# Performance work log

Measured on AMD Instinct MI355X. Metric: run time of the kernel, lower is better.

Reference implementation:

```python
import jax, jax.numpy as jnp
import numpy as np

B, N = 64, 4096          # trees per batch, leaves per complete binary tree
V, S = 21, 50            # amino-acid vocab, grammar-symbol vocab
E, H = 64, 128           # embed_dim, hidden_dim


def setup_inputs() -> dict:
    key = jax.random.key(0)
    ks = jax.random.split(key, 16)

    def lin_w(k, din, dout):
        return (jax.random.normal(k, (dout, din), jnp.float32) / np.sqrt(din)).astype(jnp.float32)

    tokens = jax.random.randint(ks[0], (B, N), 0, V, dtype=jnp.int32)
    symbols = jax.random.randint(ks[1], (B, N - 1), 0, S, dtype=jnp.int32)

    emb = jax.random.normal(ks[2], (V, E), jnp.float32) * 0.02
    emb = emb.at[0].set(0.0)  # padding_idx=0
    sym_emb = jax.random.normal(ks[3], (S, E), jnp.float32) * 0.02

    return {
        "tokens": tokens, "symbols": symbols,
        "emb": emb, "sym_emb": sym_emb,
        "Wp": lin_w(ks[4], E, H), "bp": jnp.zeros((H,), jnp.float32),
        "Wi": lin_w(ks[5], H, H), "bi": jnp.zeros((H,), jnp.float32),
        "Ui": lin_w(ks[6], H, H),
        "Wf": lin_w(ks[7], H, H), "bf": jnp.zeros((H,), jnp.float32),
        "Uf": lin_w(ks[8], H, H),
        "Wo": lin_w(ks[9], H, H), "bo": jnp.zeros((H,), jnp.float32),
        "Uo": lin_w(ks[10], H, H),
        "Wu": lin_w(ks[11], H, H), "bu": jnp.zeros((H,), jnp.float32),
        "Uu": lin_w(ks[12], H, H),
        "Wout": lin_w(ks[13], H, H), "bout": jnp.zeros((H,), jnp.float32),
    }


def _encode(tokens, symbols, emb, sym_emb, Wp, bp, Wi, bi, Ui, Wf, bf, Uf,
            Wo, bo, Uo, Wu, bu, Uu, Wout, bout):
    emb = emb.at[0].set(0.0)  # padding row contributes nothing (and gets no grad)

    # Leaf nodes: amino-acid embedding -> input_proj, no children.
    x = emb[tokens] @ Wp.T + bp                      # [B, N, H]
    i = jax.nn.sigmoid(x @ Wi.T + bi)
    o = jax.nn.sigmoid(x @ Wo.T + bo)
    u = jnp.tanh(x @ Wu.T + bu)
    c = i * u                                        # [B, N, H]
    h = o * jnp.tanh(c)

    # Bottom-up over levels of the complete binary tree (Child-Sum Tree-LSTM).
    off, n = 0, N
    while n > 1:
        m = n // 2
        xs = sym_emb[symbols[:, off:off + m]] @ Wp.T + bp   # [B, m, H]
        hl, hr = h[:, 0::2], h[:, 1::2]
        cl, cr = c[:, 0::2], c[:, 1::2]
        ht = hl + hr                                         # h_tilde = sum_j h_j
        gi = jax.nn.sigmoid(xs @ Wi.T + bi + ht @ Ui.T)
        go = jax.nn.sigmoid(xs @ Wo.T + bo + ht @ Uo.T)
        gu = jnp.tanh(xs @ Wu.T + bu + ht @ Uu.T)
        fx = xs @ Wf.T + bf
        fl = jax.nn.sigmoid(fx + hl @ Uf.T)                  # per-child forget gates
        fr = jax.nn.sigmoid(fx + hr @ Uf.T)
        c = gi * gu + fl * cl + fr * cr
        h = go * jnp.tanh(c)
        off += m
        n = m

    root_h = h[:, 0]                                         # [B, H]
    return root_h @ Wout.T + bout                            # output_proj


def reference(tokens, symbols, emb, sym_emb, Wp, bp, Wi, bi, Ui, Wf, bf, Uf,
              Wo, bo, Uo, Wu, bu, Uu, Wout, bout):
    return _encode(tokens, symbols, emb, sym_emb, Wp, bp, Wi, bi, Ui, Wf, bf,
                   Uf, Wo, bo, Uo, Wu, bu, Uu, Wout, bout)
```

## Files before the change

### kernel.cpp

```cpp
#include <hip/hip_runtime.h>
#include <hip/hip_bf16.h>

typedef __attribute__((ext_vector_type(8))) short short8;
typedef __attribute__((ext_vector_type(4))) float f32x4;

static constexpr int B_ = 64;
static constexpr int N_ = 4096;
static constexpr int V_ = 21;
static constexpr int S_ = 50;
static constexpr int E_ = 64;
static constexpr int H_ = 128;
static constexpr int NPAIR = V_ * V_;
static constexpr int NTAB = NPAIR * S_;

__device__ __forceinline__ float rcp_(float x) { return __builtin_amdgcn_rcpf(x); }
__device__ __forceinline__ float sigm(float x) { return rcp_(1.0f + __expf(-x)); }
__device__ __forceinline__ float tanh_(float x) {
  float a = fabsf(x);
  float e = __expf(-2.0f * a);
  float t = (1.0f - e) * rcp_(1.0f + e);
  return x < 0.0f ? -t : t;
}
__device__ __forceinline__ unsigned short f2bf(float f) {
  __hip_bfloat16 b = __float2bfloat16(f);
  return *reinterpret_cast<unsigned short*>(&b);
}
__device__ __forceinline__ float bf2f(unsigned short u) {
  return __uint_as_float(((unsigned int)u) << 16);
}

struct Gates { float cv, hv; };
__device__ __forceinline__ Gates gate_combine(float4 sx,
    float i_p, float o_p, float u_p, float fl_p, float fr_p, float cl, float cr) {
  float gi = sigm(sx.x + i_p);
  float go = sigm(sx.y + o_p);
  float gu = tanh_(sx.z + u_p);
  float fl = sigm(sx.w + fl_p);
  float fr = sigm(sx.w + fr_p);
  float cv = fmaf(gi, gu, fmaf(fl, cl, fr * cr));
  Gates g; g.cv = cv; g.hv = go * tanh_(cv);
  return g;
}

__device__ __forceinline__ void bar_lds() {
  asm volatile("s_waitcnt lgkmcnt(0)" ::: "memory");
  __builtin_amdgcn_s_barrier();
  asm volatile("" ::: "memory");
}
__device__ __forceinline__ void bar_only() {
  asm volatile("" ::: "memory");
  __builtin_amdgcn_s_barrier();
  asm volatile("" ::: "memory");
}

__global__ void __launch_bounds__(512) k_pre0(
    const float* __restrict__ Ui, const float* __restrict__ Uo,
    const float* __restrict__ Uu, const float* __restrict__ Uf,
    const float* __restrict__ Wi, const float* __restrict__ Wo,
    const float* __restrict__ Wu, const float* __restrict__ Wf,
    const float* __restrict__ Wp, const float* __restrict__ Wout,
    unsigned short* __restrict__ Wfrag, float* __restrict__ Wt,
    float* __restrict__ Wxt, float* __restrict__ Wpt,
    float* __restrict__ Woutt) {
  __shared__ float Tt[32][129];
  int blk = blockIdx.x, t = threadIdx.x;
  if (blk < 16) {
    int idx = blk * 512 + t;
    int L = idx & 63;
    int K = (idx >> 6) & 3;
    int T = idx >> 8;
    int n = 16 * T + (L & 15);
    int k0 = 32 * K + ((L >> 4) << 3);
    int g = n >> 7, o = n & 127;
    const float* U = (g == 0) ? Ui : (g == 1) ? Uo : (g == 2) ? Uu : Uf;
    unsigned short out[8];
    #pragma unroll
    for (int j = 0; j < 8; ++j) out[j] = f2bf(U[o * 128 + k0 + j]);
    *(int4*)(Wfrag + (size_t)idx * 8) = *(int4*)out;
  } else if (blk < 48) {
    int job = blk - 16;
    int m = job >> 2, kt = job & 3;
    int k0 = kt * 32;
    const float* M = (m == 0) ? Ui : (m == 1) ? Uo : (m == 2) ? Uu : (m == 3) ? Uf
                   : (m == 4) ? Wi : (m == 5) ? Wo : (m == 6) ? Wu : Wf;
    float* D = (m < 4) ? Wt : Wxt;
    int g = m & 3;
    #pragma unroll
    for (int pass = 0; pass < 2; ++pass) {
      int o = (t >> 3) + 64 * pass;
      int kk = 4 * (t & 7);
      float4 v = *(const float4*)(M + o * 128 + k0 + kk);
      Tt[kk][o] = v.x; Tt[kk + 1][o] = v.y; Tt[kk + 2][o] = v.z; Tt[kk + 3][o] = v.w;
    }
    __syncthreads();
    #pragma unroll
    for (int pass = 0; pass < 8; ++pass) {
      int kk = pass * 4 + (t >> 7);
      int o = t & 127;
      D[(size_t)(k0 + kk) * 512 + g * 128 + o] = Tt[kk][o];
    }
  } else if (blk == 48) {
    for (int i = t; i < E_ * H_; i += 512) {
      int e = i >> 7, o = i & 127;
      Wpt[i] = Wp[o * E_ + e];
    }
  } else {
    for (int i = t; i < H_ * H_; i += 512) {
      int k = i >> 7, o = i & 127;
      Woutt[i] = Wout[o * H_ + k];
    }
  }
}

__global__ void __launch_bounds__(512) k_pre1(
    const float* __restrict__ emb, const float* __restrict__ sym_emb,
    const float* __restrict__ Wpt, const float* __restrict__ Wxt,
    const float* __restrict__ Wt,
    const float* __restrict__ bp, const float* __restrict__ bi,
    const float* __restrict__ bo, const float* __restrict__ bu,
    const float* __restrict__ bfv,
    float* __restrict__ leaf_c, float* __restrict__ symx,
    float* __restrict__ P_leaf) {
  __shared__ float x[128];
  __shared__ float zs[512];
  __shared__ float hl[128];
  int blk = blockIdx.x, t = threadIdx.x;
  if (blk < V_) {
    int v = blk;
    if (t < 128) {
      float acc = bp[t];
      if (v != 0) {
        for (int e = 0; e < E_; ++e) acc = fmaf(emb[v * E_ + e], Wpt[e * 128 + t], acc);
      }
      x[t] = acc;
    }
    __syncthreads();
    if (t < 384) {
      int g = t >> 7;
      const float* bb = (g == 0) ? bi : (g == 1) ? bo : bu;
      float z = bb[t & 127];
      for (int k = 0; k < H_; ++k) z = fmaf(x[k], Wxt[k * 512 + t], z);
      zs[t] = z;
    }
    __syncthreads();
    if (t < 128) {
      float gi = sigm(zs[t]), go = sigm(zs[128 + t]), gu = tanh_(zs[256 + t]);
      float c = gi * gu;
      leaf_c[v * H_ + t] = c;
      unsigned short hb = f2bf(go * tanh_(c));
      hl[t] = bf2f(hb);
    }
    __syncthreads();
    {
      float z = 0.f;
      for (int k = 0; k < H_; ++k) z = fmaf(hl[k], Wt[k * 512 + t], z);
      P_leaf[(size_t)v * 512 + t] = z;
    }
  } else {
    int s = blk - V_;
    if (t < 128) {
      float acc = bp[t];
      for (int e = 0; e < E_; ++e) acc = fmaf(sym_emb[s * E_ + e], Wpt[e * 128 + t], acc);
      x[t] = acc;
    }
    __syncthreads();
    {
      int g = t >> 7;
      const float* bb = (g == 0) ? bi : (g == 1) ? bo : (g == 2) ? bu : bfv;
      float z = bb[t & 127];
      for (int k = 0; k < H_; ++k) z = fmaf(x[k], Wxt[k * 512 + t], z);
      zs[t] = z;
    }
    __syncthreads();
    if (t < 128) {
      float4 v4 = make_float4(zs[t], zs[128 + t], zs[256 + t], zs[384 + t]);
      *(float4*)(symx + (size_t)s * 512 + t * 4) = v4;
    }
  }
}

__global__ void k_tabB(const float* __restrict__ P_leaf, const float* __restrict__ symx,
                       const float* __restrict__ leaf_c,
                       const int* __restrict__ tokens, const int* __restrict__ symbols,
                       unsigned short* __restrict__ tab_h8, float* __restrict__ tab_c,
                       int* __restrict__ idx1) {
  int blk = blockIdx.x, t = threadIdx.x;
  if (blk < NTAB / 2) {
    int row = blk * 2 + (t >> 7);
    int u = t & 127;
    int p = row / S_, s = row - p * S_;
    int tl = p / V_, tr = p - tl * V_;
    const float* Pl = P_leaf + (size_t)tl * 512;
    const float* Pr = P_leaf + (size_t)tr * 512;
    float4 sx = *(const float4*)(symx + (size_t)s * 512 + u * 4);
    Gates gt = gate_combine(sx,
        Pl[u] + Pr[u], Pl[128 + u] + Pr[128 + u], Pl[256 + u] + Pr[256 + u],
        Pl[384 + u], Pr[384 + u],
        leaf_c[tl * H_ + u], leaf_c[tr * H_ + u]);
    tab_c[(size_t)row * H_ + u] = gt.cv;
    tab_h8[(size_t)row * H_ + u] = f2bf(gt.hv);
  } else {
    int g = (blk - NTAB / 2) * 256 + t;
    int b = g >> 11, j = g & 2047;
    idx1[g] = (tokens[b * N_ + 2 * j] * V_ + tokens[b * N_ + 2 * j + 1]) * S_ + symbols[b * (N_ - 1) + j];
  }
}

__global__ void __launch_bounds__(512) k_lvl23(
    const unsigned short* __restrict__ Wfrag, const float* __restrict__ symx,
    const int* __restrict__ symbols, const int* __restrict__ idx1,
    const unsigned short* __restrict__ gh8, const float* __restrict__ gc,
    unsigned short* __restrict__ h_out8, float* __restrict__ c_out) {
  __shared__ __align__(16) unsigned short Ag[32][136];
  __shared__ __align__(16) unsigned short Bh[16][136];
  __shared__ float Bc[16][132];
  const int t = threadIdx.x;
  const int w = t >> 6, L = t & 63, q = L >> 4, cL = L & 15;
  const int cc = 16 * w + cL;
  const int rowA = t >> 4, coA = (t & 15) * 8;

  const short8* wf = (const short8*)Wfrag;
  short8 bfr[4][4];
  #pragma unroll
  for (int K = 0; K < 4; ++K)
    #pragma unroll
    for (int g = 0; g < 4; ++g)
      bfr[g][K] = wf[(size_t)((w + 8 * g) * 4 + K) * 64 + L];

  const int CH = 8;
  const int t0 = blockIdx.x * CH;

  int nn[4];
  #pragma unroll
  for (int it = 0; it < 4; ++it) nn[it] = 8 * (it >> 1) + 2 * q + (it & 1);

  int gxr = idx1[t0 * 32 + rowA];
  int4 agv = *(const int4*)(gh8 + (size_t)gxr * H_ + coA);
  int g2l[4], g2r[4], sp1[4];
  {
    const int* sb = symbols + (size_t)(t0 >> 6) * (N_ - 1);
    const int j20 = (t0 & 63) * 16;
    #pragma unroll
    for (int it = 0; it < 4; ++it) {
      g2l[it] = idx1[t0 * 32 + 2 * nn[it]];
      g2r[it] = idx1[t0 * 32 + 2 * nn[it] + 1];
      sp1[it] = sb[2048 + j20 + nn[it]];
    }
  }

  for (int k = 0; k < CH; ++k) {
    const int tile = t0 + k;
    const int j2 = (tile & 63) * 16;
    const int* sb = symbols + (size_t)(tile >> 6) * (N_ - 1);

    bar_only();
    *(int4*)&Ag[rowA][coA] = agv;
    bar_lds();

    float clp[4], crp[4];
    #pragma unroll
    for (int it = 0; it < 4; ++it) {
      clp[it] = gc[(size_t)g2l[it] * H_ + cc];
      crp[it] = gc[(size_t)g2r[it] * H_ + cc];
    }
    int gxr_n = 0, g2l_n[4], g2r_n[4], sp1_n[4];
    if (k + 1 < CH) {
      const int tn = tile + 1;
      const int* sbn = symbols + (size_t)(tn >> 6) * (N_ - 1);
      const int j2n = (tn & 63) * 16;
      gxr_n = idx1[tn * 32 + rowA];
      #pragma unroll
      for (int it = 0; it < 4; ++it) {
        g2l_n[it] = idx1[tn * 32 + 2 * nn[it]];
        g2r_n[it] = idx1[tn * 32 + 2 * nn[it] + 1];
        sp1_n[it] = sbn[2048 + j2n + nn[it]];
      }
    }
    int sp2[2];
    sp2[0] = sb[3072 + (j2 >> 1) + 2 * q];
    sp2[1] = sb[3072 + (j2 >> 1) + 2 * q + 1];

    f32x4 acc[2][4];
    #pragma unroll
    for (int r = 0; r < 2; ++r)
      #pragma unroll
      for (int g = 0; g < 4; ++g) acc[r][g] = (f32x4){0.f, 0.f, 0.f, 0.f};
    #pragma unroll
    for (int K = 0; K < 4; ++K) {
      short8 a0 = *(const short8*)&Ag[cL][K * 32 + q * 8];
      short8 a1 = *(const short8*)&Ag[16 + cL][K * 32 + q * 8];
      #pragma unroll
      for (int g = 0; g < 4; ++g) {
        acc[0][g] = __builtin_amdgcn_mfma_f32_16x16x32_bf16(a0, bfr[g][K], acc[0][g], 0, 0, 0);
        acc[1][g] = __builtin_amdgcn_mfma_f32_16x16x32_bf16(a1, bfr[g][K], acc[1][g], 0, 0, 0);
      }
    }
    if (k + 1 < CH) agv = *(const int4*)(gh8 + (size_t)gxr_n * H_ + coA);

    #pragma unroll
    for (int r = 0; r < 2; ++r) {
      #pragma unroll
      for (int nd = 0; nd < 2; ++nd) {
        int it = r * 2 + nd;
        int n = 8 * r + 2 * q + nd;
        float4 sx = *(const float4*)(symx + (size_t)sp1[it] * 512 + cc * 4);
        Gates gt = gate_combine(sx,
            acc[r][0][2 * nd] + acc[r][0][2 * nd + 1],
            acc[r][1][2 * nd] + acc[r][1][2 * nd + 1],
            acc[r][2][2 * nd] + acc[r][2][2 * nd + 1],
            acc[r][3][2 * nd], acc[r][3][2 * nd + 1], clp[it], crp[it]);
        Bc[n][cc] = gt.cv;
        Bh[n][cc] = f2bf(gt.hv);
      }
    }
    bar_lds();

    f32x4 acc2[4];
    #pragma unroll
    for (int g = 0; g < 4; ++g) acc2[g] = (f32x4){0.f, 0.f, 0.f, 0.f};
    #pragma unroll
    for (int K = 0; K < 4; ++K) {
      short8 a0 = *(const short8*)&Bh[cL][K * 32 + q * 8];
      #pragma unroll
      for (int g = 0; g < 4; ++g)
        acc2[g] = __builtin_amdgcn_mfma_f32_16x16x32_bf16(a0, bfr[g][K], acc2[g], 0, 0, 0);
    }
    #pragma unroll
    for (int nd = 0; nd < 2; ++nd) {
      int n = 2 * q + nd;
      int G3 = tile * 8 + n;
      float4 sx = *(const float4*)(symx + (size_t)sp2[nd] * 512 + cc * 4);
      Gates gt = gate_combine(sx,
          acc2[0][2 * nd] + acc2[0][2 * nd + 1],
          acc2[1][2 * nd] + acc2[1][2 * nd + 1],
          acc2[2][2 * nd] + acc2[2][2 * nd + 1],
          acc2[3][2 * nd], acc2[3][2 * nd + 1],
          Bc[2 * n][cc], Bc[2 * n + 1][cc]);
      c_out[(size_t)G3 * H_ + cc] = gt.cv;
      h_out8[(size_t)G3 * H_ + cc] = f2bf(gt.hv);
    }
    gxr = gxr_n;
    #pragma unroll
    for (int it = 0; it < 4; ++it) {
      g2l[it] = g2l_n[it]; g2r[it] = g2r_n[it]; sp1[it] = sp1_n[it];
    }
  }
}

__global__ void __launch_bounds__(512, 2) k_mid(
    const unsigned short* __restrict__ Wfrag, const float* __restrict__ symx,
    const int* __restrict__ symbols,
    const unsigned short* __restrict__ in_h8, const float* __restrict__ in_c,
    unsigned short* __restrict__ out_h8, float* __restrict__ out_c) {
  __shared__ __align__(16) unsigned short Ah0[64][136];
  __shared__ __align__(16) unsigned short Ah1[32][136];
  __shared__ float Cs0[64][128];
  __shared__ float Cs1[32][128];
  int t = threadIdx.x;
  int w = t >> 6, L = t & 63, q = L >> 4, cL = L & 15;
  int cc = 16 * w + cL;
  int blk = blockIdx.x;
  int b = blk >> 3, sub = blk & 7;
  size_t base3 = (size_t)blk * 64;

  #pragma unroll
  for (int i = 0; i < 2; ++i) {
    int fid = t + 512 * i;
    int row = fid >> 4, co = (fid & 15) * 8;
    *(int4*)&Ah0[row][co] = *(const int4*)(in_h8 + (base3 + row) * H_ + co);
  }
  #pragma unroll
  for (int i = 0; i < 4; ++i) {
    int fid = t + 512 * i;
    int row = fid >> 5, c4 = (fid & 31) << 2;
    *(float4*)&Cs0[row][c4] = *(const float4*)(in_c + (base3 + row) * H_ + c4);
  }
  __syncthreads();

  const short8* wf = (const short8*)Wfrag;
  int R = 64;
  #pragma unroll
  for (int lev = 0; lev < 6; ++lev) {
    const int l = 4 + lev;
    const int nodes = R >> 1;
    const int jb = b * (N_ - 1) + (N_ - (N_ >> (l - 1))) + ((sub * 32) >> lev);
    unsigned short (*Ard)[136] = (lev & 1) ? Ah1 : Ah0;
    unsigned short (*Awr)[136] = (lev & 1) ? Ah0 : Ah1;
    const float* crd = (lev & 1) ? &Cs1[0][0] : &Cs0[0][0];
    float* cwr = (lev & 1) ? &Cs0[0][0] : &Cs1[0][0];
    const int nchunk = (nodes + 15) >> 4;
    for (int c = 0; c < nchunk; ++c) {
      int spre[4];
      #pragma unroll
      for (int it = 0; it < 4; ++it) {
        int n = 16 * c + 8 * (it >> 1) + 2 * q + (it & 1);
        spre[it] = (n < nodes) ? symbols[jb + n] : 0;
      }
      f32x4 acc[2][4];
      #pragma unroll
      for (int r = 0; r < 2; ++r)
        #pragma unroll
        for (int g = 0; g < 4; ++g) acc[r][g] = (f32x4){0.f, 0.f, 0.f, 0.f};
      const bool useA1 = (2 * nodes - 32 * c) > 16;
      #pragma unroll
      for (int K = 0; K < 4; ++K) {
        short8 bfr[4];
        #pragma unroll
        for (int g = 0; g < 4; ++g) bfr[g] = wf[(size_t)((w + 8 * g) * 4 + K) * 64 + L];
        short8 a0 = *(const short8*)&Ard[32 * c + cL][K * 32 + q * 8];
        #pragma unroll
        for (int g = 0; g < 4; ++g)
          acc[0][g] = __builtin_amdgcn_mfma_f32_16x16x32_bf16(a0, bfr[g], acc[0][g], 0, 0, 0);
        if (useA1) {
          short8 a1 = *(const short8*)&Ard[32 * c + 16 + cL][K * 32 + q * 8];
          #pragma unroll
          for (int g = 0; g < 4; ++g)
            acc[1][g] = __builtin_amdgcn_mfma_f32_16x16x32_bf16(a1, bfr[g], acc[1][g], 0, 0, 0);
        }
      }
      #pragma unroll
      for (int r = 0; r < 2; ++r) {
        #pragma unroll
        for (int nd = 0; nd < 2; ++nd) {
          int it = r * 2 + nd;
          int n = 16 * c + 8 * r + 2 * q + nd;
          if (n < nodes) {
            float4 sx = *(const float4*)(symx + (size_t)spre[it] * 512 + cc * 4);
            Gates gt = gate_combine(sx,
                acc[r][0][2 * nd] + acc[r][0][2 * nd + 1],
                acc[r][1][2 * nd] + acc[r][1][2 * nd + 1],
                acc[r][2][2 * nd] + acc[r][2][2 * nd + 1],
                acc[r][3][2 * nd], acc[r][3][2 * nd + 1],
                crd[(size_t)(2 * n) * 128 + cc], crd[(size_t)(2 * n + 1) * 128 + cc]);
            if (lev == 5) {
              out_c[(size_t)blk * H_ + cc] = gt.cv;
              out_h8[(size_t)blk * H_ + cc] = f2bf(gt.hv);
            } else {
              cwr[(size_t)n * 128 + cc] = gt.cv;
              Awr[n][cc] = f2bf(gt.hv);
            }
          }
        }
      }
    }
    __syncthreads();
    R >>= 1;
  }
}

__global__ void __launch_bounds__(512, 2) k_fin(
    const unsigned short* __restrict__ Wfrag, const float* __restrict__ symx,
    const int* __restrict__ symbols,
    const unsigned short* __restrict__ in_h8, const float* __restrict__ in_c,
    const float* __restrict__ Woutt, const float* __restrict__ bout,
    float* __restrict__ out) {
  __shared__ __align__(16) unsigned short Ah0[8][136];
  __shared__ __align__(16) unsigned short Ah1[4][136];
  __shared__ float Cs0[8][128];
  __shared__ float Cs1[4][128];
  __shared__ float rootv[128];
  int t = threadIdx.x;
  int w = t >> 6, L = t & 63, q = L >> 4, cL = L & 15;
  int cc = 16 * w + cL;
  int b = blockIdx.x;

  if (t < 128) {
    int row = t >> 4, co = (t & 15) * 8;
    *(int4*)&Ah0[row][co] = *(const int4*)(in_h8 + (size_t)(b * 8 + row) * H_ + co);
  }
  if (t < 256) {
    int row = t >> 5, c4 = (t & 31) << 2;
    *(float4*)&Cs0[row][c4] = *(const float4*)(in_c + (size_t)(b * 8 + row) * H_ + c4);
  }
  __syncthreads();

  const short8* wf = (const short8*)Wfrag;
  int R = 8;
  #pragma unroll
  for (int lev = 0; lev < 3; ++lev) {
    const int l = 10 + lev;
    const int nodes = R >> 1;
    const int jb = b * (N_ - 1) + (N_ - (N_ >> (l - 1)));
    unsigned short (*Ard)[136] = (lev & 1) ? Ah1 : Ah0;
    unsigned short (*Awr)[136] = (lev & 1) ? Ah0 : Ah1;
    const float* crd = (lev & 1) ? &Cs1[0][0] : &Cs0[0][0];
    float* cwr = (lev & 1) ? &Cs0[0][0] : &Cs1[0][0];
    int spre[4];
    #pragma unroll
    for (int it = 0; it < 4; ++it) {
      int n = 8 * (it >> 1) + 2 * q + (it & 1);
      spre[it] = (n < nodes) ? symbols[jb + n] : 0;
    }
    f32x4 acc[4];
    #pragma unroll
    for (int g = 0; g < 4; ++g) acc[g] = (f32x4){0.f, 0.f, 0.f, 0.f};
    #pragma unroll
    for (int K = 0; K < 4; ++K) {
      short8 bfr[4];
      #pragma unroll
      for (int g = 0; g < 4; ++g) bfr[g] = wf[(size_t)((w + 8 * g) * 4 + K) * 64 + L];
      short8 a0 = *(const short8*)&Ard[cL & 7][K * 32 + q * 8];
      #pragma unroll
      for (int g = 0; g < 4; ++g)
        acc[g] = __builtin_amdgcn_mfma_f32_16x16x32_bf16(a0, bfr[g], acc[g], 0, 0, 0);
    }
    #pragma unroll
    for (int nd = 0; nd < 2; ++nd) {
      int it = nd;
      int n = 2 * q + nd;
      if (n < nodes) {
        float4 sx = *(const float4*)(symx + (size_t)spre[it] * 512 + cc * 4);
        Gates gt = gate_combine(sx,
            acc[0][2 * nd] + acc[0][2 * nd + 1],
            acc[1][2 * nd] + acc[1][2 * nd + 1],
            acc[2][2 * nd] + acc[2][2 * nd + 1],
            acc[3][2 * nd], acc[3][2 * nd + 1],
            crd[(size_t)(2 * n) * 128 + cc], crd[(size_t)(2 * n + 1) * 128 + cc]);
        if (lev == 2) {
          rootv[cc] = gt.hv;
        } else {
          cwr[(size_t)n * 128 + cc] = gt.cv;
          Awr[n][cc] = f2bf(gt.hv);
        }
      }
    }
    __syncthreads();
    R >>= 1;
  }
  if (t < 128) {
    float acc = bout[t];
    for (int k = 0; k < H_; ++k) acc = fmaf(rootv[k], Woutt[k * 128 + t], acc);
    out[(size_t)b * H_ + t] = acc;
  }
}

extern "C" void kernel_launch(void* const* d_in, const int* in_sizes, int n_in,
                              void* d_out, int out_size, void* d_ws, size_t ws_size,
                              hipStream_t stream) {
  const int* tokens    = (const int*)d_in[0];
  const int* symbols   = (const int*)d_in[1];
  const float* emb     = (const float*)d_in[2];
  const float* sym_emb = (const float*)d_in[3];
  const float* Wp  = (const float*)d_in[4];
  const float* bp  = (const float*)d_in[5];
  const float* Wi  = (const float*)d_in[6];
  const float* bi  = (const float*)d_in[7];
  const float* Ui  = (const float*)d_in[8];
  const float* Wf  = (const float*)d_in[9];
  const float* bf  = (const float*)d_in[10];
  const float* Uf  = (const float*)d_in[11];
  const float* Wo  = (const float*)d_in[12];
  const float* bo  = (const float*)d_in[13];
  const float* Uo  = (const float*)d_in[14];
  const float* Wu  = (const float*)d_in[15];
  const float* bu  = (const float*)d_in[16];
  const float* Uu  = (const float*)d_in[17];
  const float* Wout= (const float*)d_in[18];
  const float* bout= (const float*)d_in[19];

  char* ws = (char*)d_ws;
  unsigned short* Wfrag   = (unsigned short*)(ws);
  float*          Wt      = (float*)(ws + 131072);
  float*          Wxt     = (float*)(ws + 393216);
  float*          Wpt     = (float*)(ws + 655360);
  float*          Woutt   = (float*)(ws + 688128);
  float*          leaf_c  = (float*)(ws + 759040);
  float*          symx    = (float*)(ws + 769792);
  float*          P_leaf  = (float*)(ws + 872192);
  unsigned short* tab_h8  = (unsigned short*)(ws + 2001152UL);
  float*          tab_c   = (float*)(ws + 7645952UL);
  int*            idx1    = (int*)(ws + 18935552UL);
  unsigned short* L3h8    = (unsigned short*)(ws + 19459840UL);
  float*          L3c     = (float*)(ws + 27848448UL);
  unsigned short* L9h8    = (unsigned short*)(ws + 44625664UL);
  float*          L9c     = (float*)(ws + 44756736UL);

  k_pre0<<<50, 512, 0, stream>>>(Ui, Uo, Uu, Uf, Wi, Wo, Wu, Wf, Wp, Wout,
                                 Wfrag, Wt, Wxt, Wpt, Woutt);
  k_pre1<<<V_ + S_, 512, 0, stream>>>(emb, sym_emb, Wpt, Wxt, Wt,
                                      bp, bi, bo, bu, bf,
                                      leaf_c, symx, P_leaf);
  k_tabB<<<NTAB / 2 + 512, 256, 0, stream>>>(P_leaf, symx, leaf_c, tokens, symbols,
                                             tab_h8, tab_c, idx1);
  k_lvl23<<<512, 512, 0, stream>>>(Wfrag, symx, symbols, idx1, tab_h8, tab_c,
                                   L3h8, L3c);
  k_mid<<<512, 512, 0, stream>>>(Wfrag, symx, symbols, L3h8, L3c, L9h8, L9c);
  k_fin<<<B_, 512, 0, stream>>>(Wfrag, symx, symbols, L9h8, L9c, Woutt, bout,
                                (float*)d_out);
}
```

Baseline: 200.4 us.

## Merge preprocessing kernels, drop weight transposes, halve lvl23 chunk, add MFMA priority

Folds the two preprocessing kernels and the idx1 computation into one launch. The transposed weight copies are removed, so the small projections now read row-major weights directly with float4 loads. k_lvl23 processes 4 chunks per block instead of 8 on twice as many blocks, and s_setprio is raised around its MFMA loops. Removing a launch and the transpose traffic cuts serial preprocessing latency, but the direct row-major reads are strided across threads, which may hurt coalescing.

```diff
diff --git a/kernel.cpp b/kernel.cpp
--- a/kernel.cpp
+++ b/kernel.cpp
@@ -53,16 +53,23 @@
   asm volatile("" ::: "memory");
 }
 
-__global__ void __launch_bounds__(512) k_pre0(
+__global__ void __launch_bounds__(512) k_pre(
     const float* __restrict__ Ui, const float* __restrict__ Uo,
     const float* __restrict__ Uu, const float* __restrict__ Uf,
     const float* __restrict__ Wi, const float* __restrict__ Wo,
     const float* __restrict__ Wu, const float* __restrict__ Wf,
-    const float* __restrict__ Wp, const float* __restrict__ Wout,
-    unsigned short* __restrict__ Wfrag, float* __restrict__ Wt,
-    float* __restrict__ Wxt, float* __restrict__ Wpt,
-    float* __restrict__ Woutt) {
-  __shared__ float Tt[32][129];
+    const float* __restrict__ Wp, const float* __restrict__ emb,
+    const float* __restrict__ sym_emb,
+    const float* __restrict__ bp, const float* __restrict__ bi,
+    const float* __restrict__ bo, const float* __restrict__ bu,
+    const float* __restrict__ bfv,
+    const int* __restrict__ tokens, const int* __restrict__ symbols,
+    unsigned short* __restrict__ Wfrag, float* __restrict__ leaf_c,
+    float* __restrict__ symx, float* __restrict__ P_leaf,
+    int* __restrict__ idx1) {
+  __shared__ float x[128];
+  __shared__ float zs[512];
+  __shared__ float hl[128];
   int blk = blockIdx.x, t = threadIdx.x;
   if (blk < 16) {
     int idx = blk * 512 + t;
@@ -77,69 +84,35 @@
     #pragma unroll
     for (int j = 0; j < 8; ++j) out[j] = f2bf(U[o * 128 + k0 + j]);
     *(int4*)(Wfrag + (size_t)idx * 8) = *(int4*)out;
-  } else if (blk < 48) {
-    int job = blk - 16;
-    int m = job >> 2, kt = job & 3;
-    int k0 = kt * 32;
-    const float* M = (m == 0) ? Ui : (m == 1) ? Uo : (m == 2) ? Uu : (m == 3) ? Uf
-                   : (m == 4) ? Wi : (m == 5) ? Wo : (m == 6) ? Wu : Wf;
-    float* D = (m < 4) ? Wt : Wxt;
-    int g = m & 3;
-    #pragma unroll
-    for (int pass = 0; pass < 2; ++pass) {
-      int o = (t >> 3) + 64 * pass;
-      int kk = 4 * (t & 7);
-      float4 v = *(const float4*)(M + o * 128 + k0 + kk);
-      Tt[kk][o] = v.x; Tt[kk + 1][o] = v.y; Tt[kk + 2][o] = v.z; Tt[kk + 3][o] = v.w;
-    }
-    __syncthreads();
-    #pragma unroll
-    for (int pass = 0; pass < 8; ++pass) {
-      int kk = pass * 4 + (t >> 7);
-      int o = t & 127;
-      D[(size_t)(k0 + kk) * 512 + g * 128 + o] = Tt[kk][o];
-    }
-  } else if (blk == 48) {
-    for (int i = t; i < E_ * H_; i += 512) {
-      int e = i >> 7, o = i & 127;
-      Wpt[i] = Wp[o * E_ + e];
-    }
-  } else {
-    for (int i = t; i < H_ * H_; i += 512) {
-      int k = i >> 7, o = i & 127;
-      Woutt[i] = Wout[o * H_ + k];
-    }
-  }
-}
-
-__global__ void __launch_bounds__(512) k_pre1(
-    const float* __restrict__ emb, const float* __restrict__ sym_emb,
-    const float* __restrict__ Wpt, const float* __restrict__ Wxt,
-    const float* __restrict__ Wt,
-    const float* __restrict__ bp, const float* __restrict__ bi,
-    const float* __restrict__ bo, const float* __restrict__ bu,
-    const float* __restrict__ bfv,
-    float* __restrict__ leaf_c, float* __restrict__ symx,
-    float* __restrict__ P_leaf) {
-  __shared__ float x[128];
-  __shared__ float zs[512];
-  __shared__ float hl[128];
-  int blk = blockIdx.x, t = threadIdx.x;
-  if (blk < V_) {
-    int v = blk;
+  } else if (blk < 16 + V_) {
+    int v = blk - 16;
     if (t < 128) {
       float acc = bp[t];
       if (v != 0) {
-        for (int e = 0; e < E_; ++e) acc = fmaf(emb[v * E_ + e], Wpt[e * 128 + t], acc);
+        const float4* wr = (const float4*)(Wp + t * E_);
+        const float4* er = (const float4*)(emb + v * E_);
+        #pragma unroll 4
+        for (int e4 = 0; e4 < E_ / 4; ++e4) {
+          float4 w4 = wr[e4], e4v = er[e4];
+          acc = fmaf(e4v.x, w4.x, acc); acc = fmaf(e4v.y, w4.y, acc);
+          acc = fmaf(e4v.z, w4.z, acc); acc = fmaf(e4v.w, w4.w, acc);
+        }
       }
       x[t] = acc;
     }
     __syncthreads();
     if (t < 384) {
-      int g = t >> 7;
+      int g = t >> 7, o = t & 127;
       const float* bb = (g == 0) ? bi : (g == 1) ? bo : bu;
-      float z = bb[t & 127];
-      for (int k = 0; k < H_; ++k) z = fmaf(x[k], Wxt[k * 512 + t], z);
+      const float* Wg = (g == 0) ? Wi : (g == 1) ? Wo : Wu;
+      float z = bb[o];
+      const float4* wr = (const float4*)(Wg + o * H_);
+      #pragma unroll 4
+      for (int k4 = 0; k4 < H_ / 4; ++k4) {
+        float4 w4 = wr[k4];
+        z = fmaf(x[4 * k4], w4.x, z); z = fmaf(x[4 * k4 + 1], w4.y, z);
+        z = fmaf(x[4 * k4 + 2], w4.z, z); z = fmaf(x[4 * k4 + 3], w4.w, z);
+      }
       zs[t] = z;
     }
     __syncthreads();
@@ -152,23 +125,45 @@
     }
     __syncthreads();
     {
+      int g = t >> 7, o = t & 127;
+      const float* Ug = (g == 0) ? Ui : (g == 1) ? Uo : (g == 2) ? Uu : Uf;
       float z = 0.f;
-      for (int k = 0; k < H_; ++k) z = fmaf(hl[k], Wt[k * 512 + t], z);
+      const float4* wr = (const float4*)(Ug + o * H_);
+      #pragma unroll 4
+      for (int k4 = 0; k4 < H_ / 4; ++k4) {
+        float4 w4 = wr[k4];
+        z = fmaf(hl[4 * k4], w4.x, z); z = fmaf(hl[4 * k4 + 1], w4.y, z);
+        z = fmaf(hl[4 * k4 + 2], w4.z, z); z = fmaf(hl[4 * k4 + 3], w4.w, z);
+      }
       P_leaf[(size_t)v * 512 + t] = z;
     }
-  } else {
-    int s = blk - V_;
+  } else if (blk < 16 + V_ + S_) {
+    int s = blk - 16 - V_;
     if (t < 128) {
       float acc = bp[t];
-      for (int e = 0; e < E_; ++e) acc = fmaf(sym_emb[s * E_ + e], Wpt[e * 128 + t], acc);
+      const float4* wr = (const float4*)(Wp + t * E_);
+      const float4* er = (const float4*)(sym_emb + s * E_);
+      #pragma unroll 4
+      for (int e4 = 0; e4 < E_ / 4; ++e4) {
+        float4 w4 = wr[e4], e4v = er[e4];
+        acc = fmaf(e4v.x, w4.x, acc); acc = fmaf(e4v.y, w4.y, acc);
+        acc = fmaf(e4v.z, w4.z, acc); acc = fmaf(e4v.w, w4.w, acc);
+      }
       x[t] = acc;
     }
     __syncthreads();
     {
-      int g = t >> 7;
+      int g = t >> 7, o = t & 127;
       const float* bb = (g == 0) ? bi : (g == 1) ? bo : (g == 2) ? bu : bfv;
-      float z = bb[t & 127];
-      for (int k = 0; k < H_; ++k) z = fmaf(x[k], Wxt[k * 512 + t], z);
+      const float* Wg = (g == 0) ? Wi : (g == 1) ? Wo : (g == 2) ? Wu : Wf;
+      float z = bb[o];
+      const float4* wr = (const float4*)(Wg + o * H_);
+      #pragma unroll 4
+      for (int k4 = 0; k4 < H_ / 4; ++k4) {
+        float4 w4 = wr[k4];
+        z = fmaf(x[4 * k4], w4.x, z); z = fmaf(x[4 * k4 + 1], w4.y, z);
+        z = fmaf(x[4 * k4 + 2], w4.z, z); z = fmaf(x[4 * k4 + 3], w4.w, z);
+      }
       zs[t] = z;
     }
     __syncthreads();
@@ -176,34 +171,31 @@
       float4 v4 = make_float4(zs[t], zs[128 + t], zs[256 + t], zs[384 + t]);
       *(float4*)(symx + (size_t)s * 512 + t * 4) = v4;
     }
+  } else {
+    int g = (blk - 16 - V_ - S_) * 512 + t;
+    int b = g >> 11, j = g & 2047;
+    idx1[g] = (tokens[b * N_ + 2 * j] * V_ + tokens[b * N_ + 2 * j + 1]) * S_
+              + symbols[b * (N_ - 1) + j];
   }
 }
 
 __global__ void k_tabB(const float* __restrict__ P_leaf, const float* __restrict__ symx,
                        const float* __restrict__ leaf_c,
-                       const int* __restrict__ tokens, const int* __restrict__ symbols,
-                       unsigned short* __restrict__ tab_h8, float* __restrict__ tab_c,
-                       int* __restrict__ idx1) {
+                       unsigned short* __restrict__ tab_h8, float* __restrict__ tab_c) {
   int blk = blockIdx.x, t = threadIdx.x;
-  if (blk < NTAB / 2) {
-    int row = blk * 2 + (t >> 7);
-    int u = t & 127;
-    int p = row / S_, s = row - p * S_;
-    int tl = p / V_, tr = p - tl * V_;
-    const float* Pl = P_leaf + (size_t)tl * 512;
-    const float* Pr = P_leaf + (size_t)tr * 512;
-    float4 sx = *(const float4*)(symx + (size_t)s * 512 + u * 4);
-    Gates gt = gate_combine(sx,
-        Pl[u] + Pr[u], Pl[128 + u] + Pr[128 + u], Pl[256 + u] + Pr[256 + u],
-        Pl[384 + u], Pr[384 + u],
-        leaf_c[tl * H_ + u], leaf_c[tr * H_ + u]);
-    tab_c[(size_t)row * H_ + u] = gt.cv;
-    tab_h8[(size_t)row * H_ + u] = f2bf(gt.hv);
-  } else {
-    int g = (blk - NTAB / 2) * 256 + t;
-    int b = g >> 11, j = g & 2047;
-    idx1[g] = (tokens[b * N_ + 2 * j] * V_ + tokens[b * N_ + 2 * j + 1]) * S_ + symbols[b * (N_ - 1) + j];
-  }
+  int row = blk * 2 + (t >> 7);
+  int u = t & 127;
+  int p = row / S_, s = row - p * S_;
+  int tl = p / V_, tr = p - tl * V_;
+  const float* Pl = P_leaf + (size_t)tl * 512;
+  const float* Pr = P_leaf + (size_t)tr * 512;
+  float4 sx = *(const float4*)(symx + (size_t)s * 512 + u * 4);
+  Gates gt = gate_combine(sx,
+      Pl[u] + Pr[u], Pl[128 + u] + Pr[128 + u], Pl[256 + u] + Pr[256 + u],
+      Pl[384 + u], Pr[384 + u],
+      leaf_c[tl * H_ + u], leaf_c[tr * H_ + u]);
+  tab_c[(size_t)row * H_ + u] = gt.cv;
+  tab_h8[(size_t)row * H_ + u] = f2bf(gt.hv);
 }
 
 __global__ void __launch_bounds__(512) k_lvl23(
@@ -227,7 +219,7 @@
     for (int g = 0; g < 4; ++g)
       bfr[g][K] = wf[(size_t)((w + 8 * g) * 4 + K) * 64 + L];
 
-  const int CH = 8;
+  const int CH = 4;
   const int t0 = blockIdx.x * CH;
 
   int nn[4];
@@ -285,6 +277,7 @@
     for (int r = 0; r < 2; ++r)
       #pragma unroll
       for (int g = 0; g < 4; ++g) acc[r][g] = (f32x4){0.f, 0.f, 0.f, 0.f};
+    __builtin_amdgcn_s_setprio(1);
     #pragma unroll
     for (int K = 0; K < 4; ++K) {
       short8 a0 = *(const short8*)&Ag[cL][K * 32 + q * 8];
@@ -295,6 +288,7 @@
         acc[1][g] = __builtin_amdgcn_mfma_f32_16x16x32_bf16(a1, bfr[g][K], acc[1][g], 0, 0, 0);
       }
     }
+    __builtin_amdgcn_s_setprio(0);
     if (k + 1 < CH) agv = *(const int4*)(gh8 + (size_t)gxr_n * H_ + coA);
 
     #pragma unroll
@@ -318,6 +312,7 @@
     f32x4 acc2[4];
     #pragma unroll
     for (int g = 0; g < 4; ++g) acc2[g] = (f32x4){0.f, 0.f, 0.f, 0.f};
+    __builtin_amdgcn_s_setprio(1);
     #pragma unroll
     for (int K = 0; K < 4; ++K) {
       short8 a0 = *(const short8*)&Bh[cL][K * 32 + q * 8];
@@ -325,6 +320,7 @@
       for (int g = 0; g < 4; ++g)
         acc2[g] = __builtin_amdgcn_mfma_f32_16x16x32_bf16(a0, bfr[g][K], acc2[g], 0, 0, 0);
     }
+    __builtin_amdgcn_s_setprio(0);
     #pragma unroll
     for (int nd = 0; nd < 2; ++nd) {
       int n = 2 * q + nd;
@@ -452,7 +448,7 @@
     const unsigned short* __restrict__ Wfrag, const float* __restrict__ symx,
     const int* __restrict__ symbols,
     const unsigned short* __restrict__ in_h8, const float* __restrict__ in_c,
-    const float* __restrict__ Woutt, const float* __restrict__ bout,
+    const float* __restrict__ Wout, const float* __restrict__ bout,
     float* __restrict__ out) {
   __shared__ __align__(16) unsigned short Ah0[8][136];
   __shared__ __align__(16) unsigned short Ah1[4][136];
@@ -529,7 +525,13 @@
   }
   if (t < 128) {
     float acc = bout[t];
-    for (int k = 0; k < H_; ++k) acc = fmaf(rootv[k], Woutt[k * 128 + t], acc);
+    const float4* wr = (const float4*)(Wout + t * H_);
+    #pragma unroll 4
+    for (int k4 = 0; k4 < H_ / 4; ++k4) {
+      float4 w4 = wr[k4];
+      acc = fmaf(rootv[4 * k4], w4.x, acc); acc = fmaf(rootv[4 * k4 + 1], w4.y, acc);
+      acc = fmaf(rootv[4 * k4 + 2], w4.z, acc); acc = fmaf(rootv[4 * k4 + 3], w4.w, acc);
+    }
     out[(size_t)b * H_ + t] = acc;
   }
 }
@@ -560,10 +562,6 @@
 
   char* ws = (char*)d_ws;
   unsigned short* Wfrag   = (unsigned short*)(ws);
-  float*          Wt      = (float*)(ws + 131072);
-  float*          Wxt     = (float*)(ws + 393216);
-  float*          Wpt     = (float*)(ws + 655360);
-  float*          Woutt   = (float*)(ws + 688128);
   float*          leaf_c  = (float*)(ws + 759040);
   float*          symx    = (float*)(ws + 769792);
   float*          P_leaf  = (float*)(ws + 872192);
@@ -575,16 +573,14 @@
   unsigned short* L9h8    = (unsigned short*)(ws + 44625664UL);
   float*          L9c     = (float*)(ws + 44756736UL);
 
-  k_pre0<<<50, 512, 0, stream>>>(Ui, Uo, Uu, Uf, Wi, Wo, Wu, Wf, Wp, Wout,
-                                 Wfrag, Wt, Wxt, Wpt, Woutt);
-  k_pre1<<<V_ + S_, 512, 0, stream>>>(emb, sym_emb, Wpt, Wxt, Wt,
-                                      bp, bi, bo, bu, bf,
-                                      leaf_c, symx, P_leaf);
-  k_tabB<<<NTAB / 2 + 512, 256, 0, stream>>>(P_leaf, symx, leaf_c, tokens, symbols,
-                                             tab_h8, tab_c, idx1);
-  k_lvl23<<<512, 512, 0, stream>>>(Wfrag, symx, symbols, idx1, tab_h8, tab_c,
-                                   L3h8, L3c);
+  k_pre<<<16 + V_ + S_ + 256, 512, 0, stream>>>(
+      Ui, Uo, Uu, Uf, Wi, Wo, Wu, Wf, Wp, emb, sym_emb,
+      bp, bi, bo, bu, bf, tokens, symbols,
+      Wfrag, leaf_c, symx, P_leaf, idx1);
+  k_tabB<<<NTAB / 2, 256, 0, stream>>>(P_leaf, symx, leaf_c, tab_h8, tab_c);
+  k_lvl23<<<1024, 512, 0, stream>>>(Wfrag, symx, symbols, idx1, tab_h8, tab_c,
+                                    L3h8, L3c);
   k_mid<<<512, 512, 0, stream>>>(Wfrag, symx, symbols, L3h8, L3c, L9h8, L9c);
-  k_fin<<<B_, 512, 0, stream>>>(Wfrag, symx, symbols, L9h8, L9c, Woutt, bout,
+  k_fin<<<B_, 512, 0, stream>>>(Wfrag, symx, symbols, L9h8, L9c, Wout, bout,
                                 (float*)d_out);
 }
```

Measured after the change: 204.1 us. No clear change (+1.9%).
